# Optimization experiments

Measured on AMD Instinct MI355X. Metric: run time of the kernel, lower is better.

Reference implementation:

```python
import jax, jax.numpy as jnp
import numpy as np

N = 100000
E = 1600000
F_IN, HID, N_CLS = 128, 16, 32


def setup_inputs() -> dict:
    key = jax.random.key(0)
    ks = jax.random.split(key, 10)
    x = jax.random.normal(ks[0], (N, F_IN), dtype=jnp.float32)
    edge_index = jax.random.randint(ks[1], (2, E), 0, N, dtype=jnp.int64)
    edge_weight = jax.random.uniform(ks[2], (E,), dtype=jnp.float32)
    def glorot(k, shape):
        lim = np.sqrt(6.0 / (shape[0] + shape[1])).astype(np.float32)
        return jax.random.uniform(k, shape, dtype=jnp.float32, minval=-lim, maxval=lim)
    return {
        'x': x, 'edge_index': edge_index, 'edge_weight': edge_weight,
        'W1_0': glorot(ks[3], (F_IN, HID)), 'W1_1': glorot(ks[4], (F_IN, HID)),
        'b1': jnp.zeros((HID,), jnp.float32),
        'W2_0': glorot(ks[5], (HID, N_CLS)), 'W2_1': glorot(ks[6], (HID, N_CLS)),
        'b2': jnp.zeros((N_CLS,), jnp.float32),
    }


def _cheb_conv_k2(x, row, col, edge_weight, W0, W1, b):
    # PyG ChebConv, K=2, lambda_max=2.0:
    #   T0 = x; T1 = L_hat x = D^{-1/2} A D^{-1/2} x - x
    n = x.shape[0]
    deg = jax.ops.segment_sum(edge_weight, row, num_segments=n)  # [N]
    dinv = jnp.where(deg > 0, jax.lax.rsqrt(deg), 0.0)
    norm = dinv[row] * edge_weight * dinv[col]                   # [E]
    agg = jax.ops.segment_sum(norm[:, None] * x[col], row, num_segments=n)  # [N,F]
    tx1 = agg - x
    return x @ W0 + tx1 @ W1 + b


def reference(x, edge_index, edge_weight, W1_0, W1_1, b1, W2_0, W2_1, b2):
    row, col = edge_index[0], edge_index[1]
    h = jax.nn.relu(_cheb_conv_k2(x, row, col, edge_weight, W1_0, W1_1, b1))
    # dropout(p=0) and DFA layers are identity in forward
    out = _cheb_conv_k2(h, row, col, edge_weight, W2_0, W2_1, b2)
    return jax.nn.log_softmax(out, axis=1)
```

## Files before the change

kernel.cpp:

```cpp
#include <hip/hip_runtime.h>
#include <hip/hip_bf16.h>


#include <hip/hip_fp16.h>

constexpr int NN   = 100000;
constexpr int NE   = 1600000;
constexpr int FIN  = 128;
constexpr int HID  = 16;
constexpr int NCLS = 32;

constexpr int RB    = 256;
constexpr int NBKT  = (NN + RB - 1) / RB;
constexpr int EPB   = 4096;
constexpr int EPT   = EPB / 256;
constexpr int GP    = (NE + EPB - 1) / EPB;
constexpr int CAP   = 8192;
constexpr int NTILE = NN / 16;
constexpr int NPAIR = NN / 2;

typedef float f32x2 __attribute__((ext_vector_type(2)));
typedef float f32x4 __attribute__((ext_vector_type(4)));
typedef short bf16x8 __attribute__((ext_vector_type(8)));

#if defined(__has_builtin)
#if __has_builtin(__builtin_amdgcn_cvt_pk_f32_fp8)
#define HAVE_CVT_FP8 1
#endif
#endif

static __device__ __forceinline__ unsigned int f2e4m3(float f) {
    union { float f; unsigned int u; } v; v.f = f;
    unsigned int s = (v.u >> 24) & 0x80u;
    unsigned int au = v.u & 0x7fffffffu;
    if (au > 0x43E00000u) au = 0x43E00000u;
    au += 0x7ffffu + ((au >> 20) & 1u);
    int e4 = (int)(au >> 23) - 120;
    unsigned int m = (au >> 20) & 7u;
    unsigned int byte = (e4 <= 0) ? 0u : (((unsigned int)e4 << 3) | m);
    return s | byte;
}
static __device__ __forceinline__ void fp8x4_fma(unsigned int v, float w, float* acc) {
#ifdef HAVE_CVT_FP8
    f32x2 lo = __builtin_amdgcn_cvt_pk_f32_fp8((int)v, false);
    f32x2 hi = __builtin_amdgcn_cvt_pk_f32_fp8((int)v, true);
    acc[0] += w * lo.x; acc[1] += w * lo.y;
    acc[2] += w * hi.x; acc[3] += w * hi.y;
#else
#pragma unroll
    for (int i = 0; i < 4; i++) {
        unsigned int b = (v >> (8 * i)) & 0xffu;
        float f = __int_as_float((int)(((b & 0x80u) << 24) | ((b & 0x7fu) << 20))) * 0x1p120f;
        acc[i] += w * f;
    }
#endif
}
static __device__ __forceinline__ unsigned short f2bf(float f) {
    union { float f; unsigned int u; } v; v.f = f;
    unsigned int r = v.u + 0x7fffu + ((v.u >> 16) & 1u);
    return (unsigned short)(r >> 16);
}
static __device__ __forceinline__ unsigned int wpack(float wf) {
    unsigned int b = __float_as_uint(wf) + 0x8000u;
    return (b >> 16) & 0x7fffu;
}
static __device__ __forceinline__ float wdec(unsigned int u) {
    return __uint_as_float((u >> 17) << 16);
}

__global__ void k_zero_cur(int* __restrict__ bucketCursor) {
    int i = blockIdx.x * blockDim.x + threadIdx.x;
    if (i < NBKT) bucketCursor[i] = 0;
}

__global__ __launch_bounds__(256) void k_partition(
    const int* __restrict__ row, const int* __restrict__ col,
    const float* __restrict__ w, int* __restrict__ bucketCursor,
    int2* __restrict__ partS) {
    __shared__ int2 stage[EPB];
    __shared__ unsigned short sbkt[EPB];
    __shared__ int cnt[NBKT];
    __shared__ int lofs[NBKT];
    __shared__ int cursor[NBKT];
    __shared__ int gbase[NBKT];
    __shared__ int sa[512], sb[512];
    int tid = threadIdx.x;
    long ebase = (long)blockIdx.x * EPB;
    int rr[EPT]; int cc[EPT]; float wv[EPT];
#pragma unroll
    for (int i = 0; i < EPT; i++) {
        long e = ebase + i * 256 + tid;
        if (e < NE) { rr[i] = row[e]; cc[i] = col[e]; wv[i] = w[e]; }
        else rr[i] = -1;
    }
    for (int i = tid; i < NBKT; i += 256) cnt[i] = 0;
    __syncthreads();
#pragma unroll
    for (int i = 0; i < EPT; i++)
        if (rr[i] >= 0) atomicAdd(&cnt[rr[i] >> 8], 1);
    __syncthreads();
    for (int i = tid; i < 512; i += 256) sa[i] = (i < NBKT) ? cnt[i] : 0;
    __syncthreads();
    int* src = sa; int* dst = sb;
    for (int off = 1; off < 512; off <<= 1) {
        for (int i = tid; i < 512; i += 256)
            dst[i] = src[i] + ((i >= off) ? src[i - off] : 0);
        __syncthreads();
        int* t = src; src = dst; dst = t;
    }
    for (int i = tid; i < NBKT; i += 256) {
        int ex = src[i] - cnt[i];
        lofs[i] = ex;
        cursor[i] = ex;
        int go = (cnt[i] > 0) ? atomicAdd(&bucketCursor[i], cnt[i]) : 0;
        gbase[i] = i * CAP + go;
    }
    __syncthreads();
#pragma unroll
    for (int i = 0; i < EPT; i++) {
        if (rr[i] >= 0) {
            int b = rr[i] >> 8;
            int p = atomicAdd(&cursor[b], 1);
            int2 v;
            v.x = cc[i] | ((rr[i] & 255) << 17);
            v.y = __float_as_int(wv[i]);
            stage[p] = v;
            sbkt[p] = (unsigned short)b;
        }
    }
    __syncthreads();
    int total = (int)min((long)EPB, NE - ebase);
    for (int i = tid; i < total; i += 256) {
        int b = sbkt[i];
        partS[gbase[b] + (i - lofs[b])] = stage[i];
    }
}

__global__ __launch_bounds__(256) void k_bucket_sort(
    const int2* __restrict__ partS, const int* __restrict__ bucketCursor,
    unsigned int* __restrict__ partC, int* __restrict__ rowptr,
    float* __restrict__ dinv) {
    __shared__ int hist[RB];
    __shared__ int cursor[RB];
    __shared__ float dsum[RB];
    __shared__ int wtot[4];
    __shared__ int red[4];
    int b = blockIdx.x;
    int tid = threadIdx.x;
    int lane = tid & 63, wv = tid >> 6;
    int partial = 0;
    for (int i = tid; i < b; i += 256) partial += bucketCursor[i];
#pragma unroll
    for (int off = 1; off < 64; off <<= 1) partial += __shfl_xor(partial, off, 64);
    if (lane == 0) red[wv] = partial;
    hist[tid] = 0;
    dsum[tid] = 0.f;
    __syncthreads();
    int start = red[0] + red[1] + red[2] + red[3];
    int count = bucketCursor[b];
    const int2* src = partS + (long)b * CAP;
    for (int i = tid; i < count; i += 256)
        atomicAdd(&hist[((unsigned)src[i].x >> 17) & 255], 1);
    __syncthreads();
    int v = hist[tid];
    int sc = v;
#pragma unroll
    for (int off = 1; off < 64; off <<= 1) {
        int up = __shfl_up(sc, off, 64);
        if (lane >= off) sc += up;
    }
    if (lane == 63) wtot[wv] = sc;
    __syncthreads();
    int add = 0;
    for (int w2 = 0; w2 < wv; w2++) add += wtot[w2];
    int ex = sc + add - v;
    int node = b * RB + tid;
    if (node <= NN) rowptr[node] = start + ex;
    cursor[tid] = ex;
    __syncthreads();
    for (int i = tid; i < count; i += 256) {
        int2 p = src[i];
        int rl = ((unsigned)p.x >> 17) & 255;
        int pos = atomicAdd(&cursor[rl], 1);
        float wf = __int_as_float(p.y);
        partC[start + pos] = ((unsigned)p.x & 0x1FFFFu) | (wpack(wf) << 17);
        atomicAdd(&dsum[rl], wf);
    }
    __syncthreads();
    if (node < NN) {
        float dsv = dsum[tid];
        dinv[node] = dsv > 0.f ? rsqrtf(dsv) : 0.f;
    }
}

__global__ __launch_bounds__(256) void k_proj1(
    const float* __restrict__ x, const float* __restrict__ W0,
    const float* __restrict__ W1, const float* __restrict__ b1,
    const float* __restrict__ dinv,
    float* __restrict__ xa, unsigned char* __restrict__ xb8) {
    int wid = (int)(((long)blockIdx.x * 256 + threadIdx.x) >> 6);
    if (wid >= NTILE) return;
    int lane = threadIdx.x & 63;
    int col = lane & 15, quad = lane >> 4;

    bf16x8 bfrag[2][4];
#pragma unroll
    for (int mat = 0; mat < 2; mat++) {
        const float* W = mat ? W1 : W0;
#pragma unroll
        for (int kb = 0; kb < 4; kb++) {
            bf16x8 f;
#pragma unroll
            for (int j = 0; j < 8; j++)
                f[j] = (short)f2bf(W[(kb * 32 + quad * 8 + j) * HID + col]);
            bfrag[mat][kb] = f;
        }
    }

    const float* xrow = x + ((long)wid * 16 + col) * FIN + quad * 8;
    float4 xb[8];
#pragma unroll
    for (int kb = 0; kb < 4; kb++) {
        xb[2 * kb]     = *(const float4*)(xrow + kb * 32);
        xb[2 * kb + 1] = *(const float4*)(xrow + kb * 32 + 4);
    }
    f32x4 acc0 = {0.f, 0.f, 0.f, 0.f}, acc1 = {0.f, 0.f, 0.f, 0.f};
#pragma unroll
    for (int kb = 0; kb < 4; kb++) {
        float4 a0 = xb[2 * kb], a1 = xb[2 * kb + 1];
        bf16x8 af;
        af[0] = (short)f2bf(a0.x); af[1] = (short)f2bf(a0.y);
        af[2] = (short)f2bf(a0.z); af[3] = (short)f2bf(a0.w);
        af[4] = (short)f2bf(a1.x); af[5] = (short)f2bf(a1.y);
        af[6] = (short)f2bf(a1.z); af[7] = (short)f2bf(a1.w);
        acc0 = __builtin_amdgcn_mfma_f32_16x16x32_bf16(af, bfrag[0][kb], acc0, 0, 0, 0);
        acc1 = __builtin_amdgcn_mfma_f32_16x16x32_bf16(af, bfrag[1][kb], acc1, 0, 0, 0);
    }

    float b1v = b1[col];
#pragma unroll
    for (int r = 0; r < 4; r++) {
        long node = (long)wid * 16 + quad * 4 + r;
        float a0 = acc0[r], a1 = acc1[r];
        xa[node * HID + col] = a0 - a1 + b1v;
        float dn = dinv[node];
        xb8[node * HID + col] = (unsigned char)f2e4m3(dn * a1);
    }
}

static __device__ __forceinline__ void proj2_epi(
    long n, int lane, float dn, const float4 xav, const float* acc,
    const float* __restrict__ W0, const float* __restrict__ W1,
    const float* __restrict__ b2, float* __restrict__ ha,
    unsigned char* __restrict__ hb8) {
    float hq0 = fmaxf(xav.x + dn * acc[0], 0.f);
    float hq1 = fmaxf(xav.y + dn * acc[1], 0.f);
    float hq2 = fmaxf(xav.z + dn * acc[2], 0.f);
    float hq3 = fmaxf(xav.w + dn * acc[3], 0.f);
    float h[16];
#pragma unroll
    for (int a = 0; a < 4; a++) {
        h[4 * a + 0] = __shfl(hq0, a, 64);
        h[4 * a + 1] = __shfl(hq1, a, 64);
        h[4 * a + 2] = __shfl(hq2, a, 64);
        h[4 * a + 3] = __shfl(hq3, a, 64);
    }
    int m = lane >> 5, o = lane & 31;
    const float* Wm = m ? W1 : W0;
    float acc2 = 0.f;
#pragma unroll
    for (int k = 0; k < HID; k++) acc2 += h[k] * Wm[k * NCLS + o];
    float other = __shfl_xor(acc2, 32);
    if (m == 0) {
        ha[n * NCLS + o] = acc2 - other + b2[o];
    } else {
        unsigned int c0 = f2e4m3(dn * acc2);
        unsigned int c1 = __shfl_down(c0, 1);
        unsigned int c2 = __shfl_down(c0, 2);
        unsigned int c3 = __shfl_down(c0, 3);
        if ((o & 3) == 0)
            *(unsigned int*)(hb8 + n * NCLS + o) =
                c0 | (c1 << 8) | (c2 << 16) | (c3 << 24);
    }
}

__global__ __launch_bounds__(256) void k_gather1_proj2(
    const int* __restrict__ rowptr, const unsigned int* __restrict__ partC,
    const float* __restrict__ dinv, const unsigned char* __restrict__ xb8,
    const float* __restrict__ xa, const float* __restrict__ W0,
    const float* __restrict__ W1, const float* __restrict__ b2,
    float* __restrict__ ha, unsigned char* __restrict__ hb8) {
    long t = (long)blockIdx.x * 256 + threadIdx.x;
    int w = (int)(t >> 6);
    if (w >= NPAIR) return;
    int lane = threadIdx.x & 63;
    int d = lane & 3, p = lane >> 2;
    long n0 = (long)w * 2, n1 = n0 + 1;

    int s0 = rowptr[n0], e0 = rowptr[n0 + 1], e1 = rowptr[n0 + 2];
    float2 dnv = *(const float2*)(dinv + n0);
    float4 xav0 = *(const float4*)(xa + n0 * HID + d * 4);
    float4 xav1 = *(const float4*)(xa + n1 * HID + d * 4);

    float acc0[4] = {0.f, 0.f, 0.f, 0.f};
    float acc1[4] = {0.f, 0.f, 0.f, 0.f};
    int j0 = s0 + p, j1 = e0 + p;
    while ((j0 < e0) | (j1 < e1)) {
        if (j0 < e0) {
            unsigned int u = partC[j0];
            unsigned int v = *(const unsigned int*)(xb8 + (u & 0x1FFFF) * HID + d * 4);
            fp8x4_fma(v, wdec(u), acc0);
            j0 += 16;
        }
        if (j1 < e1) {
            unsigned int u = partC[j1];
            unsigned int v = *(const unsigned int*)(xb8 + (u & 0x1FFFF) * HID + d * 4);
            fp8x4_fma(v, wdec(u), acc1);
            j1 += 16;
        }
    }
#pragma unroll
    for (int i = 0; i < 4; i++) {
        acc0[i] += __shfl_xor(acc0[i], 4);  acc1[i] += __shfl_xor(acc1[i], 4);
        acc0[i] += __shfl_xor(acc0[i], 8);  acc1[i] += __shfl_xor(acc1[i], 8);
        acc0[i] += __shfl_xor(acc0[i], 16); acc1[i] += __shfl_xor(acc1[i], 16);
        acc0[i] += __shfl_xor(acc0[i], 32); acc1[i] += __shfl_xor(acc1[i], 32);
    }
    proj2_epi(n0, lane, dnv.x, xav0, acc0, W0, W1, b2, ha, hb8);
    proj2_epi(n1, lane, dnv.y, xav1, acc1, W0, W1, b2, ha, hb8);
}

static __device__ __forceinline__ void lsm_epi(
    long n, int lane, float dn, const float4 hv, const float* acc,
    float* __restrict__ out) {
    int d = lane & 7, p = lane >> 3;
    float v0 = dn * acc[0] + hv.x;
    float v1 = dn * acc[1] + hv.y;
    float v2 = dn * acc[2] + hv.z;
    float v3 = dn * acc[3] + hv.w;
    float m = fmaxf(fmaxf(v0, v1), fmaxf(v2, v3));
    m = fmaxf(m, __shfl_xor(m, 1));
    m = fmaxf(m, __shfl_xor(m, 2));
    m = fmaxf(m, __shfl_xor(m, 4));
    float sum = __expf(v0 - m) + __expf(v1 - m) + __expf(v2 - m) + __expf(v3 - m);
    sum += __shfl_xor(sum, 1);
    sum += __shfl_xor(sum, 2);
    sum += __shfl_xor(sum, 4);
    float ls = logf(sum);
    if (p == 0) {
        float4 o; o.x = v0 - m - ls; o.y = v1 - m - ls;
        o.z = v2 - m - ls; o.w = v3 - m - ls;
        *(float4*)(out + n * NCLS + d * 4) = o;
    }
}

__global__ __launch_bounds__(256) void k_gather2_lsm(
    const int* __restrict__ rowptr, const unsigned int* __restrict__ partC,
    const float* __restrict__ dinv, const float* __restrict__ ha,
    const unsigned char* __restrict__ hb8, float* __restrict__ out) {
    long t = (long)blockIdx.x * 256 + threadIdx.x;
    int w = (int)(t >> 6);
    if (w >= NPAIR) return;
    int lane = threadIdx.x & 63;
    int d = lane & 7, p = lane >> 3;
    long n0 = (long)w * 2, n1 = n0 + 1;

    int s0 = rowptr[n0], e0 = rowptr[n0 + 1], e1 = rowptr[n0 + 2];
    float2 dnv = *(const float2*)(dinv + n0);
    float4 hv0 = *(const float4*)(ha + n0 * NCLS + d * 4);
    float4 hv1 = *(const float4*)(ha + n1 * NCLS + d * 4);

    float acc0[4] = {0.f, 0.f, 0.f, 0.f};
    float acc1[4] = {0.f, 0.f, 0.f, 0.f};
    int j0 = s0 + p, j1 = e0 + p;
    while ((j0 < e0) | (j1 < e1)) {
        if (j0 < e0) {
            unsigned int u = partC[j0];
            unsigned int v = *(const unsigned int*)(hb8 + (u & 0x1FFFF) * NCLS + d * 4);
            fp8x4_fma(v, wdec(u), acc0);
            j0 += 8;
        }
        if (j1 < e1) {
            unsigned int u = partC[j1];
            unsigned int v = *(const unsigned int*)(hb8 + (u & 0x1FFFF) * NCLS + d * 4);
            fp8x4_fma(v, wdec(u), acc1);
            j1 += 8;
        }
    }
#pragma unroll
    for (int i = 0; i < 4; i++) {
        acc0[i] += __shfl_xor(acc0[i], 8);  acc1[i] += __shfl_xor(acc1[i], 8);
        acc0[i] += __shfl_xor(acc0[i], 16); acc1[i] += __shfl_xor(acc1[i], 16);
        acc0[i] += __shfl_xor(acc0[i], 32); acc1[i] += __shfl_xor(acc1[i], 32);
    }
    lsm_epi(n0, lane, dnv.x, hv0, acc0, out);
    lsm_epi(n1, lane, dnv.y, hv1, acc1, out);
}

extern "C" void kernel_launch(void* const* d_in, const int* in_sizes, int n_in,
                              void* d_out, int out_size, void* d_ws, size_t ws_size,
                              hipStream_t stream) {
    const float* x    = (const float*)d_in[0];
    const int*   ei   = (const int*)d_in[1];
    const float* ew   = (const float*)d_in[2];
    const float* W1_0 = (const float*)d_in[3];
    const float* W1_1 = (const float*)d_in[4];
    const float* b1   = (const float*)d_in[5];
    const float* W2_0 = (const float*)d_in[6];
    const float* W2_1 = (const float*)d_in[7];
    const float* b2   = (const float*)d_in[8];
    float* out = (float*)d_out;

    const int* row = ei;
    const int* col = ei + NE;

    char* ws = (char*)d_ws;
    int2*  partS     = (int2*)ws;                 ws += sizeof(int2) * (long)NBKT * CAP;
    unsigned int* partC = (unsigned int*)ws;      ws += sizeof(int) * NE;
    int*   bucketCursor = (int*)ws;               ws += sizeof(int) * NBKT;
    int*   rowptr    = (int*)ws;                  ws += sizeof(int) * (NN + 4);
    float* dinv      = (float*)ws;                ws += sizeof(float) * NN;
    float* xa        = (float*)ws;                ws += sizeof(float) * NN * HID;
    float* ha        = (float*)ws;                ws += sizeof(float) * NN * NCLS;
    unsigned char* xb8 = (unsigned char*)ws;      ws += sizeof(char) * NN * HID;
    unsigned char* hb8 = (unsigned char*)ws;      ws += sizeof(char) * NN * NCLS;

    k_zero_cur<<<(NBKT + 255) / 256, 256, 0, stream>>>(bucketCursor);
    k_partition<<<GP, 256, 0, stream>>>(row, col, ew, bucketCursor, partS);
    k_bucket_sort<<<NBKT, 256, 0, stream>>>(partS, bucketCursor, partC, rowptr, dinv);
    k_proj1<<<(NTILE * 64 + 255) / 256, 256, 0, stream>>>(x, W1_0, W1_1, b1, dinv, xa, xb8);
    {
        long th = (long)NPAIR * 64;
        k_gather1_proj2<<<(int)((th + 255) / 256), 256, 0, stream>>>(
            rowptr, partC, dinv, xb8, xa, W2_0, W2_1, b2, ha, hb8);
    }
    {
        long th = (long)NPAIR * 64;
        k_gather2_lsm<<<(int)((th + 255) / 256), 256, 0, stream>>>(rowptr, partC, dinv, ha, hb8, out);
    }
}
```

Baseline: 234.6 us.

## Aggregate layer-2 in 16-dim hidden space before projecting, add MFMA lsm kernel

Reorders the second ChebConv so the neighbour aggregation runs on the 16-wide hidden features (fp8) instead of the 32-wide projected features, and then applies the projection (W0-W1 on h, W1 on the aggregate) with a bf16 MFMA in a new log-softmax kernel. This halves the bytes gathered per edge in the second sparse pass and drops the fp32 ha buffer. In exchange it adds a kernel launch and extra bf16 intermediates, and stores h and the aggregate in bf16, which changes rounding.

```diff
diff --git a/kernel.cpp b/kernel.cpp
--- a/kernel.cpp
+++ b/kernel.cpp
@@ -59,6 +59,10 @@
     union { float f; unsigned int u; } v; v.f = f;
     unsigned int r = v.u + 0x7fffu + ((v.u >> 16) & 1u);
     return (unsigned short)(r >> 16);
+}
+static __device__ __forceinline__ float bf2f(unsigned short b) {
+    union { unsigned int u; float f; } v; v.u = ((unsigned int)b) << 16;
+    return v.f;
 }
 static __device__ __forceinline__ unsigned int wpack(float wf) {
     unsigned int b = __float_as_uint(wf) + 0x8000u;
@@ -248,48 +252,11 @@
     }
 }
 
-static __device__ __forceinline__ void proj2_epi(
-    long n, int lane, float dn, const float4 xav, const float* acc,
-    const float* __restrict__ W0, const float* __restrict__ W1,
-    const float* __restrict__ b2, float* __restrict__ ha,
-    unsigned char* __restrict__ hb8) {
-    float hq0 = fmaxf(xav.x + dn * acc[0], 0.f);
-    float hq1 = fmaxf(xav.y + dn * acc[1], 0.f);
-    float hq2 = fmaxf(xav.z + dn * acc[2], 0.f);
-    float hq3 = fmaxf(xav.w + dn * acc[3], 0.f);
-    float h[16];
-#pragma unroll
-    for (int a = 0; a < 4; a++) {
-        h[4 * a + 0] = __shfl(hq0, a, 64);
-        h[4 * a + 1] = __shfl(hq1, a, 64);
-        h[4 * a + 2] = __shfl(hq2, a, 64);
-        h[4 * a + 3] = __shfl(hq3, a, 64);
-    }
-    int m = lane >> 5, o = lane & 31;
-    const float* Wm = m ? W1 : W0;
-    float acc2 = 0.f;
-#pragma unroll
-    for (int k = 0; k < HID; k++) acc2 += h[k] * Wm[k * NCLS + o];
-    float other = __shfl_xor(acc2, 32);
-    if (m == 0) {
-        ha[n * NCLS + o] = acc2 - other + b2[o];
-    } else {
-        unsigned int c0 = f2e4m3(dn * acc2);
-        unsigned int c1 = __shfl_down(c0, 1);
-        unsigned int c2 = __shfl_down(c0, 2);
-        unsigned int c3 = __shfl_down(c0, 3);
-        if ((o & 3) == 0)
-            *(unsigned int*)(hb8 + n * NCLS + o) =
-                c0 | (c1 << 8) | (c2 << 16) | (c3 << 24);
-    }
-}
-
-__global__ __launch_bounds__(256) void k_gather1_proj2(
+__global__ __launch_bounds__(256) void k_gather1(
     const int* __restrict__ rowptr, const unsigned int* __restrict__ partC,
     const float* __restrict__ dinv, const unsigned char* __restrict__ xb8,
-    const float* __restrict__ xa, const float* __restrict__ W0,
-    const float* __restrict__ W1, const float* __restrict__ b2,
-    float* __restrict__ ha, unsigned char* __restrict__ hb8) {
+    const float* __restrict__ xa,
+    unsigned short* __restrict__ h16, unsigned char* __restrict__ h8) {
     long t = (long)blockIdx.x * 256 + threadIdx.x;
     int w = (int)(t >> 6);
     if (w >= NPAIR) return;
@@ -326,49 +293,43 @@
         acc0[i] += __shfl_xor(acc0[i], 16); acc1[i] += __shfl_xor(acc1[i], 16);
         acc0[i] += __shfl_xor(acc0[i], 32); acc1[i] += __shfl_xor(acc1[i], 32);
     }
-    proj2_epi(n0, lane, dnv.x, xav0, acc0, W0, W1, b2, ha, hb8);
-    proj2_epi(n1, lane, dnv.y, xav1, acc1, W0, W1, b2, ha, hb8);
-}
-
-static __device__ __forceinline__ void lsm_epi(
-    long n, int lane, float dn, const float4 hv, const float* acc,
-    float* __restrict__ out) {
-    int d = lane & 7, p = lane >> 3;
-    float v0 = dn * acc[0] + hv.x;
-    float v1 = dn * acc[1] + hv.y;
-    float v2 = dn * acc[2] + hv.z;
-    float v3 = dn * acc[3] + hv.w;
-    float m = fmaxf(fmaxf(v0, v1), fmaxf(v2, v3));
-    m = fmaxf(m, __shfl_xor(m, 1));
-    m = fmaxf(m, __shfl_xor(m, 2));
-    m = fmaxf(m, __shfl_xor(m, 4));
-    float sum = __expf(v0 - m) + __expf(v1 - m) + __expf(v2 - m) + __expf(v3 - m);
-    sum += __shfl_xor(sum, 1);
-    sum += __shfl_xor(sum, 2);
-    sum += __shfl_xor(sum, 4);
-    float ls = logf(sum);
     if (p == 0) {
-        float4 o; o.x = v0 - m - ls; o.y = v1 - m - ls;
-        o.z = v2 - m - ls; o.w = v3 - m - ls;
-        *(float4*)(out + n * NCLS + d * 4) = o;
-    }
-}
-
-__global__ __launch_bounds__(256) void k_gather2_lsm(
+        float h0[4], h1[4];
+        h0[0] = fmaxf(xav0.x + dnv.x * acc0[0], 0.f);
+        h0[1] = fmaxf(xav0.y + dnv.x * acc0[1], 0.f);
+        h0[2] = fmaxf(xav0.z + dnv.x * acc0[2], 0.f);
+        h0[3] = fmaxf(xav0.w + dnv.x * acc0[3], 0.f);
+        h1[0] = fmaxf(xav1.x + dnv.y * acc1[0], 0.f);
+        h1[1] = fmaxf(xav1.y + dnv.y * acc1[1], 0.f);
+        h1[2] = fmaxf(xav1.z + dnv.y * acc1[2], 0.f);
+        h1[3] = fmaxf(xav1.w + dnv.y * acc1[3], 0.f);
+        ushort4 u0, u1;
+        u0.x = f2bf(h0[0]); u0.y = f2bf(h0[1]); u0.z = f2bf(h0[2]); u0.w = f2bf(h0[3]);
+        u1.x = f2bf(h1[0]); u1.y = f2bf(h1[1]); u1.z = f2bf(h1[2]); u1.w = f2bf(h1[3]);
+        *(ushort4*)(h16 + n0 * HID + d * 4) = u0;
+        *(ushort4*)(h16 + n1 * HID + d * 4) = u1;
+        unsigned int p0 = f2e4m3(dnv.x * h0[0]) | (f2e4m3(dnv.x * h0[1]) << 8)
+                        | (f2e4m3(dnv.x * h0[2]) << 16) | (f2e4m3(dnv.x * h0[3]) << 24);
+        unsigned int p1 = f2e4m3(dnv.y * h1[0]) | (f2e4m3(dnv.y * h1[1]) << 8)
+                        | (f2e4m3(dnv.y * h1[2]) << 16) | (f2e4m3(dnv.y * h1[3]) << 24);
+        *(unsigned int*)(h8 + n0 * HID + d * 4) = p0;
+        *(unsigned int*)(h8 + n1 * HID + d * 4) = p1;
+    }
+}
+
+__global__ __launch_bounds__(256) void k_gather2(
     const int* __restrict__ rowptr, const unsigned int* __restrict__ partC,
-    const float* __restrict__ dinv, const float* __restrict__ ha,
-    const unsigned char* __restrict__ hb8, float* __restrict__ out) {
+    const float* __restrict__ dinv, const unsigned char* __restrict__ h8,
+    unsigned short* __restrict__ g16) {
     long t = (long)blockIdx.x * 256 + threadIdx.x;
     int w = (int)(t >> 6);
     if (w >= NPAIR) return;
     int lane = threadIdx.x & 63;
-    int d = lane & 7, p = lane >> 3;
+    int d = lane & 3, p = lane >> 2;
     long n0 = (long)w * 2, n1 = n0 + 1;
 
     int s0 = rowptr[n0], e0 = rowptr[n0 + 1], e1 = rowptr[n0 + 2];
     float2 dnv = *(const float2*)(dinv + n0);
-    float4 hv0 = *(const float4*)(ha + n0 * NCLS + d * 4);
-    float4 hv1 = *(const float4*)(ha + n1 * NCLS + d * 4);
 
     float acc0[4] = {0.f, 0.f, 0.f, 0.f};
     float acc1[4] = {0.f, 0.f, 0.f, 0.f};
@@ -376,25 +337,94 @@
     while ((j0 < e0) | (j1 < e1)) {
         if (j0 < e0) {
             unsigned int u = partC[j0];
-            unsigned int v = *(const unsigned int*)(hb8 + (u & 0x1FFFF) * NCLS + d * 4);
+            unsigned int v = *(const unsigned int*)(h8 + (u & 0x1FFFF) * HID + d * 4);
             fp8x4_fma(v, wdec(u), acc0);
-            j0 += 8;
+            j0 += 16;
         }
         if (j1 < e1) {
             unsigned int u = partC[j1];
-            unsigned int v = *(const unsigned int*)(hb8 + (u & 0x1FFFF) * NCLS + d * 4);
+            unsigned int v = *(const unsigned int*)(h8 + (u & 0x1FFFF) * HID + d * 4);
             fp8x4_fma(v, wdec(u), acc1);
-            j1 += 8;
+            j1 += 16;
         }
     }
 #pragma unroll
     for (int i = 0; i < 4; i++) {
+        acc0[i] += __shfl_xor(acc0[i], 4);  acc1[i] += __shfl_xor(acc1[i], 4);
         acc0[i] += __shfl_xor(acc0[i], 8);  acc1[i] += __shfl_xor(acc1[i], 8);
         acc0[i] += __shfl_xor(acc0[i], 16); acc1[i] += __shfl_xor(acc1[i], 16);
         acc0[i] += __shfl_xor(acc0[i], 32); acc1[i] += __shfl_xor(acc1[i], 32);
     }
-    lsm_epi(n0, lane, dnv.x, hv0, acc0, out);
-    lsm_epi(n1, lane, dnv.y, hv1, acc1, out);
+    if (p == 0) {
+        ushort4 u0, u1;
+        u0.x = f2bf(dnv.x * acc0[0]); u0.y = f2bf(dnv.x * acc0[1]);
+        u0.z = f2bf(dnv.x * acc0[2]); u0.w = f2bf(dnv.x * acc0[3]);
+        u1.x = f2bf(dnv.y * acc1[0]); u1.y = f2bf(dnv.y * acc1[1]);
+        u1.z = f2bf(dnv.y * acc1[2]); u1.w = f2bf(dnv.y * acc1[3]);
+        *(ushort4*)(g16 + n0 * HID + d * 4) = u0;
+        *(ushort4*)(g16 + n1 * HID + d * 4) = u1;
+    }
+}
+
+__global__ __launch_bounds__(256) void k_lsm(
+    const unsigned short* __restrict__ h16, const unsigned short* __restrict__ g16,
+    const float* __restrict__ W0, const float* __restrict__ W1,
+    const float* __restrict__ b2, float* __restrict__ out) {
+    int wid = (int)(((long)blockIdx.x * 256 + threadIdx.x) >> 6);
+    if (wid >= NTILE) return;
+    int lane = threadIdx.x & 63;
+    int col = lane & 15, quad = lane >> 4;
+
+    bf16x8 bfrag[2];
+#pragma unroll
+    for (int c = 0; c < 2; c++) {
+        bf16x8 f;
+        if (quad < 2) {
+#pragma unroll
+            for (int j = 0; j < 8; j++) {
+                int k = quad * 8 + j;
+                f[j] = (short)f2bf(W0[k * NCLS + col + 16 * c] - W1[k * NCLS + col + 16 * c]);
+            }
+        } else {
+#pragma unroll
+            for (int j = 0; j < 8; j++) {
+                int k = (quad - 2) * 8 + j;
+                f[j] = (short)f2bf(W1[k * NCLS + col + 16 * c]);
+            }
+        }
+        bfrag[c] = f;
+    }
+
+    long node_a = (long)wid * 16 + col;
+    const unsigned short* abase =
+        (quad & 2) ? (g16 + node_a * HID + (quad & 1) * 8)
+                   : (h16 + node_a * HID + (quad & 1) * 8);
+    bf16x8 af = *(const bf16x8*)abase;
+
+    f32x4 c0 = {0.f, 0.f, 0.f, 0.f}, c1 = {0.f, 0.f, 0.f, 0.f};
+    c0 = __builtin_amdgcn_mfma_f32_16x16x32_bf16(af, bfrag[0], c0, 0, 0, 0);
+    c1 = __builtin_amdgcn_mfma_f32_16x16x32_bf16(af, bfrag[1], c1, 0, 0, 0);
+
+    float b2a = b2[col], b2b = b2[col + 16];
+#pragma unroll
+    for (int r = 0; r < 4; r++) {
+        long node = (long)wid * 16 + quad * 4 + r;
+        float v0 = c0[r] + b2a;
+        float v1 = c1[r] + b2b;
+        float m = fmaxf(v0, v1);
+        m = fmaxf(m, __shfl_xor(m, 1));
+        m = fmaxf(m, __shfl_xor(m, 2));
+        m = fmaxf(m, __shfl_xor(m, 4));
+        m = fmaxf(m, __shfl_xor(m, 8));
+        float sum = __expf(v0 - m) + __expf(v1 - m);
+        sum += __shfl_xor(sum, 1);
+        sum += __shfl_xor(sum, 2);
+        sum += __shfl_xor(sum, 4);
+        sum += __shfl_xor(sum, 8);
+        float ls = logf(sum);
+        out[node * NCLS + col] = v0 - m - ls;
+        out[node * NCLS + col + 16] = v1 - m - ls;
+    }
 }
 
 extern "C" void kernel_launch(void* const* d_in, const int* in_sizes, int n_in,
@@ -421,9 +451,10 @@
     int*   rowptr    = (int*)ws;                  ws += sizeof(int) * (NN + 4);
     float* dinv      = (float*)ws;                ws += sizeof(float) * NN;
     float* xa        = (float*)ws;                ws += sizeof(float) * NN * HID;
-    float* ha        = (float*)ws;                ws += sizeof(float) * NN * NCLS;
+    unsigned short* h16 = (unsigned short*)ws;    ws += sizeof(short) * NN * HID;
+    unsigned short* g16 = (unsigned short*)ws;    ws += sizeof(short) * NN * HID;
     unsigned char* xb8 = (unsigned char*)ws;      ws += sizeof(char) * NN * HID;
-    unsigned char* hb8 = (unsigned char*)ws;      ws += sizeof(char) * NN * NCLS;
+    unsigned char* h8  = (unsigned char*)ws;      ws += sizeof(char) * NN * HID;
 
     k_zero_cur<<<(NBKT + 255) / 256, 256, 0, stream>>>(bucketCursor);
     k_partition<<<GP, 256, 0, stream>>>(row, col, ew, bucketCursor, partS);
@@ -431,11 +462,10 @@
     k_proj1<<<(NTILE * 64 + 255) / 256, 256, 0, stream>>>(x, W1_0, W1_1, b1, dinv, xa, xb8);
     {
         long th = (long)NPAIR * 64;
-        k_gather1_proj2<<<(int)((th + 255) / 256), 256, 0, stream>>>(
-            rowptr, partC, dinv, xb8, xa, W2_0, W2_1, b2, ha, hb8);
-    }
-    {
-        long th = (long)NPAIR * 64;
-        k_gather2_lsm<<<(int)((th + 255) / 256), 256, 0, stream>>>(rowptr, partC, dinv, ha, hb8, out);
-    }
-}
+        k_gather1<<<(int)((th + 255) / 256), 256, 0, stream>>>(
+            rowptr, partC, dinv, xb8, xa, h16, h8);
+        k_gather2<<<(int)((th + 255) / 256), 256, 0, stream>>>(
+            rowptr, partC, dinv, h8, g16);
+    }
+    k_lsm<<<(NTILE * 64 + 255) / 256, 256, 0, stream>>>(h16, g16, W2_0, W2_1, b2, out);
+}
```

Result: faster. 213.8 us (-8.8%).
